# Kernel optimization log

Hardware: AMD Instinct MI355X
Metric: run time of the kernel (lower is better)

## Reference

```python
import jax, jax.numpy as jnp
import numpy as np

# Model dims (match init_kwargs / module defaults)
B, D, H, E, K, DEPTH, BS = 8192, 1024, 4096, 16, 2, 2, 64
SP_EXPERT, SP_CROSS = 0.85, 0.9  # block sparsities


def _block_mask(key, n_in, n_out, sparsity):
    """Bool mask [n_in, n_out] with (BS x BS)-block structure, ~(1-sparsity) dense.
    Matches torch.rand(n_blocks_out, n_blocks_in) > sparsity, expanded to full size."""
    mb = jax.random.uniform(key, (n_out // BS, n_in // BS)) > sparsity  # [ob, ib]
    return jnp.repeat(jnp.repeat(mb.T, BS, axis=0), BS, axis=1)  # [n_in, n_out]


def setup_inputs() -> dict:
    key = jax.random.key(0)
    ks = jax.random.split(key, 12)
    x = jax.random.normal(ks[0], (B, D), dtype=jnp.float32)
    gate_w = jax.random.normal(ks[1], (DEPTH, E, D), dtype=jnp.float32) / np.sqrt(D)
    temperature = jnp.ones((DEPTH,), dtype=jnp.float32)
    w1 = jax.random.normal(ks[2], (E, D, H), dtype=jnp.float32) * 0.02
    b1 = jnp.zeros((E, H), dtype=jnp.float32)
    w2 = jax.random.normal(ks[3], (E, H, D), dtype=jnp.float32) * 0.02
    b2 = jnp.zeros((E, D), dtype=jnp.float32)
    cross_w = jax.random.normal(ks[4], (D, D), dtype=jnp.float32) * 0.02
    cross_b = jnp.zeros((D,), dtype=jnp.float32)
    mk = jax.random.split(ks[5], 2 * E + 1)
    mask1 = jnp.stack([_block_mask(mk[i], D, H, SP_EXPERT) for i in range(E)])
    mask2 = jnp.stack([_block_mask(mk[E + i], H, D, SP_EXPERT) for i in range(E)])
    cross_mask = _block_mask(mk[2 * E], D, D, SP_CROSS)
    return {"x": x, "gate_w": gate_w, "temperature": temperature,
            "w1": w1, "b1": b1, "w2": w2, "b2": b2,
            "cross_w": cross_w, "cross_b": cross_b,
            "mask1": mask1, "mask2": mask2, "cross_mask": cross_mask}


def reference(x, gate_w, temperature, w1, b1, w2, b2, cross_w, cross_b,
              mask1, mask2, cross_mask):
    n_tok = x.shape[0]
    # Only the last-depth router affects the output (x is never updated and
    # expert_outputs is re-initialized each depth iteration in the original).
    logits = jnp.einsum('bd,ed->be', x, gate_w[-1]) / temperature[-1]
    top_vals, top_idx = jax.lax.top_k(logits, K)            # [n_tok, K]
    rout_w = jax.nn.softmax(top_vals, axis=-1)
    routing = jnp.zeros((n_tok, E), x.dtype).at[
        jnp.arange(n_tok)[:, None], top_idx].set(rout_w)    # [n_tok, E]

    expert_out = jnp.zeros_like(x)
    for e in range(E):  # fixed small expert count
        h = jax.nn.silu(x @ (w1[e] * mask1[e]) + b1[e])     # [n_tok, H]
        y = h @ (w2[e] * mask2[e]) + b2[e]                  # [n_tok, D]
        expert_out = expert_out + y * routing[:, e:e + 1]
    return x + expert_out @ (cross_w * cross_mask) + cross_b
```

## Files before the change

### kernel.cpp

```cpp
#include <hip/hip_runtime.h>


#define NTOK 8192
#define DIM  1024
#define HID  4096
#define NEXP 16
#define BM   256
#define ROWS_CAP (NTOK*2 + NEXP*256)

typedef __attribute__((ext_vector_type(4))) float fx4;
typedef __attribute__((ext_vector_type(4))) unsigned int ux4;
typedef __attribute__((ext_vector_type(2))) unsigned int ux2;
typedef __attribute__((ext_vector_type(8))) short s8v;
union V16 { ux4 u; s8v s; };

__device__ __forceinline__ unsigned int f2bf(float f) {
  unsigned int u = __float_as_uint(f);
  return (u + 0x7fffu + ((u >> 16) & 1u)) >> 16;
}

__device__ __forceinline__ unsigned int cvt_pk(float lo, float hi) {
  unsigned int r;
  asm("v_cvt_pk_bf16_f32 %0, %1, %2" : "=v"(r) : "v"(lo), "v"(hi));
  return r;
}

__device__ __forceinline__ unsigned int f2fp8(float v) {
  return (unsigned int)__builtin_amdgcn_cvt_pk_fp8_f32(v, v, 0, false) & 0xFFu;
}

__device__ __forceinline__ unsigned int pk4fp8(float a, float b, float c, float d) {
  unsigned int u = (unsigned int)__builtin_amdgcn_cvt_pk_fp8_f32(a, b, 0, false);
  u = (unsigned int)__builtin_amdgcn_cvt_pk_fp8_f32(c, d, (int)u, true);
  return u;
}

__device__ __forceinline__ bool mask_at(const void* m, int flag, size_t idx) {
  if (flag == 0) return ((const unsigned char*)m)[idx] != 0;
  if (flag == 1) return ((const int*)m)[idx] != 0;
  return ((const float*)m)[idx] != 0.0f;
}

__device__ __forceinline__ int flag_of(int ev) {
  return (ev & 2) ? 2 : ((ev & 1) ? 0 : 1);
}

__device__ __forceinline__ int xcd_swz() {
  const int b = blockIdx.x, cpx = gridDim.x >> 3;
  return (b & 7) * cpx + (b >> 3);
}

__device__ __forceinline__ void region_of(const int* __restrict__ meta, int base,
                                          int& e, int& rstart, int& ecnt, int& total) {
  e = 15; rstart = 0; ecnt = 0; total = 0;
  #pragma unroll
  for (int i = 0; i < 16; i++) {
    const int craw = meta[8 + i];
    const int c = (craw + 255) & ~255;
    if (base >= total && base < total + c) { e = i; rstart = total; ecnt = craw; }
    total += c;
  }
}

__global__ void k_route(const float* __restrict__ x,
                        const float* __restrict__ gw,
                        const float* __restrict__ temp,
                        const unsigned int* __restrict__ m1raw,
                        int* __restrict__ top2i, float* __restrict__ top2w,
                        int* __restrict__ meta, unsigned char* __restrict__ x8)
{
  if (blockIdx.x < 64) {
    int bits = 0;
    size_t base = (size_t)blockIdx.x * 4096 + threadIdx.x;
    for (int j = 0; j < 16; j++) {
      unsigned int v = m1raw[base + 256 * j];
      if (v == 0x3f800000u) bits |= 2;
      else if (v > 1u)      bits |= 1;
    }
    if (bits) atomicOr(&meta[1], bits);
  }

  __shared__ float gwsh[NEXP * DIM];
  for (int i = threadIdx.x; i < NEXP * DIM; i += 256) gwsh[i] = gw[i];
  __syncthreads();

  const int wv = threadIdx.x >> 6;
  const int l = threadIdx.x & 63;
  #pragma unroll
  for (int tt = 0; tt < 8; tt++) {
    const int t = blockIdx.x * 32 + wv * 8 + tt;
    const float* xr = x + (size_t)t * DIM;
    float xv[16];
    #pragma unroll
    for (int j = 0; j < 16; j++) xv[j] = xr[l + 64 * j];
    float logit[16];
    #pragma unroll
    for (int e = 0; e < 16; e++) {
      const float* g = gwsh + e * DIM;
      float s = 0.f;
      #pragma unroll
      for (int j = 0; j < 16; j++) s += xv[j] * g[l + 64 * j];
      #pragma unroll
      for (int o = 32; o >= 1; o >>= 1) s += __shfl_xor(s, o);
      logit[e] = s;
    }
    if (l == 0) {
      const float tinv = 1.0f / temp[0];
      int i0 = 0; float v0 = logit[0] * tinv;
      #pragma unroll
      for (int e = 1; e < 16; e++) { float v = logit[e] * tinv; if (v > v0) { v0 = v; i0 = e; } }
      int i1 = -1; float v1 = 0.f; bool first = true;
      #pragma unroll
      for (int e = 0; e < 16; e++) {
        if (e == i0) continue;
        float v = logit[e] * tinv;
        if (first || v > v1) { v1 = v; i1 = e; first = false; }
      }
      float ex = __expf(v1 - v0);
      float den = 1.0f + ex;
      top2i[2 * t] = i0; top2i[2 * t + 1] = i1;
      top2w[2 * t] = 1.0f / den; top2w[2 * t + 1] = ex / den;
      atomicAdd(&meta[8 + i0], 1);
      atomicAdd(&meta[8 + i1], 1);
    }
  }

  {
    const size_t be = (size_t)blockIdx.x * 32 * DIM;
    const fx4* src = (const fx4*)(x + be);
    ux4* dst = (ux4*)(x8 + be);
    #pragma unroll
    for (int i = 0; i < 8; i++) {
      const int idx = i * 256 + threadIdx.x;
      fx4 a = src[4 * idx], b = src[4 * idx + 1];
      fx4 c = src[4 * idx + 2], d = src[4 * idx + 3];
      ux4 o;
      o[0] = pk4fp8(a[0] * 16.f, a[1] * 16.f, a[2] * 16.f, a[3] * 16.f);
      o[1] = pk4fp8(b[0] * 16.f, b[1] * 16.f, b[2] * 16.f, b[3] * 16.f);
      o[2] = pk4fp8(c[0] * 16.f, c[1] * 16.f, c[2] * 16.f, c[3] * 16.f);
      o[3] = pk4fp8(d[0] * 16.f, d[1] * 16.f, d[2] * 16.f, d[3] * 16.f);
      dst[idx] = o;
    }
  }
}

__global__ void k_wcast(const float* __restrict__ w1, const float* __restrict__ w2,
                        const void* __restrict__ mask1, const void* __restrict__ mask2,
                        const int* __restrict__ meta,
                        unsigned char* __restrict__ w1p, unsigned char* __restrict__ w2p)
{
  const int flag = flag_of(meta[1]);
  const int gid = blockIdx.x;
  const int tid = threadIdx.x;
  const int c = tid >> 6, col = tid & 63;

  if (gid < 16384) {
    const int p = gid >> 4, kb = gid & 15;
    const int e = p >> 6, ct = p & 63;
    if (!mask_at(mask1, flag, (size_t)e * DIM * HID + (size_t)kb * 64 * HID + ct * 64)) return;
    const float* src = w1 + ((size_t)e * DIM + kb * 64 + c * 16) * HID + ct * 64 + col;
    ux4 v;
    #pragma unroll
    for (int q = 0; q < 4; q++) {
      float f0 = src[(size_t)(q * 4 + 0) * HID], f1 = src[(size_t)(q * 4 + 1) * HID];
      float f2 = src[(size_t)(q * 4 + 2) * HID], f3 = src[(size_t)(q * 4 + 3) * HID];
      v[q] = pk4fp8(f0 * 16.f, f1 * 16.f, f2 * 16.f, f3 * 16.f);
    }
    *(ux4*)(w1p + ((size_t)gid << 12) + col * 64 + ((c ^ ((col >> 1) & 3)) << 4)) = v;
  } else {
    const int g2 = gid - 16384;
    const int p = g2 >> 6, kb = g2 & 63;
    const int e = p >> 4, ct = p & 15;
    if (!mask_at(mask2, flag, (size_t)e * HID * DIM + (size_t)kb * 64 * DIM + ct * 64)) return;
    const float* src = w2 + ((size_t)e * HID + kb * 64 + c * 16) * DIM + ct * 64 + col;
    ux4 v;
    #pragma unroll
    for (int q = 0; q < 4; q++) {
      float f0 = src[(size_t)(q * 4 + 0) * DIM], f1 = src[(size_t)(q * 4 + 1) * DIM];
      float f2 = src[(size_t)(q * 4 + 2) * DIM], f3 = src[(size_t)(q * 4 + 3) * DIM];
      v[q] = pk4fp8(f0 * 16.f, f1 * 16.f, f2 * 16.f, f3 * 16.f);
    }
    *(ux4*)(w2p + ((size_t)g2 << 12) + col * 64 + ((c ^ ((col >> 1) & 3)) << 4)) = v;
  }
}

__global__ void k_assign(const int* __restrict__ top2i,
                         const float* __restrict__ top2w,
                         int* __restrict__ meta, int* __restrict__ tok_of_row,
                         int* __restrict__ t2row)
{
  __shared__ int offs[16];
  if (threadIdx.x < 16) {
    int o = 0;
    for (int i = 0; i < (int)threadIdx.x; i++) o += (meta[8 + i] + 255) & ~255;
    offs[threadIdx.x] = o;
  }
  __syncthreads();
  int t = blockIdx.x * 256 + threadIdx.x;
  if (t >= NTOK) return;
  #pragma unroll
  for (int k = 0; k < 2; k++) {
    int e = top2i[2 * t + k];
    int slot = atomicAdd(&meta[64 + e], 1);
    int row = offs[e] + slot;
    tok_of_row[row] = t;
    t2row[2 * t + k] = row;
  }
}

__global__ __launch_bounds__(256, 4)
void k_gemm1(const unsigned char* __restrict__ x8,
             const unsigned char* __restrict__ w1p, const float* __restrict__ b1,
             const void* __restrict__ mask1,
             const int* __restrict__ meta, const int* __restrict__ tok_of_row,
             unsigned char* __restrict__ h8)
{
  __shared__ ux4 Ash[2][1024];
  __shared__ __align__(16) unsigned int Bsh[2][1024];

  const int bid = xcd_swz();
  const int rt = bid >> 6, ct = bid & 63;
  const int base = rt * BM;
  int e, rstart, ecnt, total;
  region_of(meta, base, e, rstart, ecnt, total);
  if (base >= total) return;

  const int tid = threadIdx.x;
  const int wv = tid >> 6;
  const int jg0 = ct * 64;
  const int l = tid & 63, l16 = l & 15, lhi = l >> 4;

  unsigned int bits;
  {
    const int flag = flag_of(meta[1]);
    bool on = false;
    if (l < 16)
      on = mask_at(mask1, flag, (size_t)e * DIM * HID + (size_t)l * 64 * HID + jg0);
    bits = (unsigned int)(__ballot(on) & 0xFFFFull);
  }

  const unsigned int sw = (unsigned int)((tid & 3) ^ ((tid >> 3) & 3));
  const int vlimit = rstart + ecnt;
  unsigned int aoff[4];
  #pragma unroll
  for (int i = 0; i < 4; i++) {
    const int r = base + i * 64 + (tid >> 2);
    int tok = tok_of_row[r];
    if (r >= vlimit) tok = 0;
    aoff[i] = (unsigned int)tok * (unsigned int)DIM + sw * 16;
  }

  fx4 acc[4][4] = {};

  auto STAGE_A = [&](int b, int d0) {
    const char* gp = (const char*)x8 + d0;
    #pragma unroll
    for (int i = 0; i < 4; i++)
      __builtin_amdgcn_global_load_lds(
        (const __attribute__((address_space(1))) unsigned int*)(gp + aoff[i]),
        (__attribute__((address_space(3))) unsigned int*)&Ash[b][i * 256 + wv * 64],
        16, 0, 0);
  };
  auto STAGE_B = [&](int b, int kb) {
    const char* src = (const char*)w1p + (((size_t)(e * 64 + ct) * 16 + kb) << 12) + tid * 16;
    __builtin_amdgcn_global_load_lds(
      (const __attribute__((address_space(1))) unsigned int*)src,
      (__attribute__((address_space(3))) unsigned int*)&Bsh[b][wv * 256],
      16, 0, 0);
  };
  auto COMPUTE = [&](int b) {
    const char* Ab = (const char*)&Ash[b][0];
    const char* Bb = (const char*)&Bsh[b][0];
    #pragma unroll
    for (int ks = 0; ks < 2; ks++) {
      const int c = ks * 2 + (lhi >> 1);
      const int sub = (lhi & 1) << 3;
      long long a[4], bb[4];
      #pragma unroll
      for (int m = 0; m < 4; m++) {
        const int row = wv * 64 + m * 16 + l16;
        a[m] = *(const long long*)(Ab + row * 64 + ((c ^ ((row >> 1) & 3)) << 4) + sub);
      }
      #pragma unroll
      for (int n = 0; n < 4; n++) {
        const int col = n * 16 + l16;
        bb[n] = *(const long long*)(Bb + col * 64 + ((c ^ ((col >> 1) & 3)) << 4) + sub);
      }
      #pragma unroll
      for (int m = 0; m < 4; m++)
        #pragma unroll
        for (int n = 0; n < 4; n++)
          acc[m][n] = __builtin_amdgcn_mfma_f32_16x16x32_fp8_fp8(a[m], bb[n], acc[m][n], 0, 0, 0);
    }
  };

  if (bits) {
    int kb0 = __ffs(bits) - 1; bits &= bits - 1;
    STAGE_A(0, kb0 << 6); STAGE_B(0, kb0);
    __syncthreads();
    int cur = 0;
    for (;;) {
      int nkb = -1;
      if (bits) { nkb = __ffs(bits) - 1; bits &= bits - 1; }
      if (nkb >= 0) { STAGE_A(cur ^ 1, nkb << 6); STAGE_B(cur ^ 1, nkb); }
      COMPUTE(cur);
      __syncthreads();
      cur ^= 1;
      if (nkb < 0) break;
    }
  }

  unsigned char* hs = (unsigned char*)&Ash[0][0];
  __syncthreads();
  #pragma unroll
  for (int m = 0; m < 4; m++)
    #pragma unroll
    for (int n = 0; n < 4; n++) {
      const int gcol = jg0 + n * 16 + l16;
      const float bbv = b1[e * HID + gcol];
      #pragma unroll
      for (int i = 0; i < 4; i++) {
        const int row = wv * 64 + m * 16 + lhi * 4 + i;
        float v = acc[m][n][i] * 0.00390625f + bbv;
        float hval = v / (1.0f + __expf(-v));
        hs[row * 64 + n * 16 + l16] = (unsigned char)f2fp8(hval * 8.0f);
      }
    }
  __syncthreads();
  {
    const ux4* s = (const ux4*)hs;
    #pragma unroll
    for (int j = 0; j < 4; j++) {
      const int c2 = j * 256 + tid;
      const int row = c2 >> 2;
      *(ux4*)(h8 + (size_t)(base + row) * HID + ct * 64 + (c2 & 3) * 16) = s[c2];
    }
  }
}

__global__ __launch_bounds__(256, 4)
void k_gemm2(const unsigned char* __restrict__ h8,
             const unsigned char* __restrict__ w2p, const float* __restrict__ b2,
             const void* __restrict__ mask2,
             const int* __restrict__ meta, unsigned short* __restrict__ yb)
{
  __shared__ ux4 Ash[2][1024];
  __shared__ __align__(16) unsigned int Bsh[2][1024];

  const int bid = xcd_swz();
  const int rt = bid >> 4, ct = bid & 15;
  const int base = rt * BM;
  int e, rstart, ecnt, total;
  region_of(meta, base, e, rstart, ecnt, total);
  if (base >= total) return;

  const int tid = threadIdx.x;
  const int wv = tid >> 6;
  const int jg0 = ct * 64;

  const int l = tid & 63, l16 = l & 15, lhi = l >> 4;
  unsigned long long bits;
  {
    const int flag = flag_of(meta[1]);
    bits = __ballot(mask_at(mask2, flag,
             (size_t)e * HID * DIM + (size_t)l * 64 * DIM + jg0));
  }

  const unsigned int sw = (unsigned int)((tid & 3) ^ ((tid >> 3) & 3));
  unsigned int aoff[4];
  #pragma unroll
  for (int i = 0; i < 4; i++)
    aoff[i] = (unsigned int)(base + i * 64 + (tid >> 2)) * (unsigned int)HID + sw * 16;

  fx4 acc[4][4] = {};

  auto STAGE_A = [&](int b, int d0) {
    const char* gp = (const char*)h8 + d0;
    #pragma unroll
    for (int i = 0; i < 4; i++)
      __builtin_amdgcn_global_load_lds(
        (const __attribute__((address_space(1))) unsigned int*)(gp + aoff[i]),
        (__attribute__((address_space(3))) unsigned int*)&Ash[b][i * 256 + wv * 64],
        16, 0, 0);
  };
  auto STAGE_B = [&](int b, int kb) {
    const char* src = (const char*)w2p + (((size_t)(e * 16 + ct) * 64 + kb) << 12) + tid * 16;
    __builtin_amdgcn_global_load_lds(
      (const __attribute__((address_space(1))) unsigned int*)src,
      (__attribute__((address_space(3))) unsigned int*)&Bsh[b][wv * 256],
      16, 0, 0);
  };
  auto COMPUTE = [&](int b) {
    const char* Ab = (const char*)&Ash[b][0];
    const char* Bb = (const char*)&Bsh[b][0];
    #pragma unroll
    for (int ks = 0; ks < 2; ks++) {
      const int c = ks * 2 + (lhi >> 1);
      const int sub = (lhi & 1) << 3;
      long long a[4], bb[4];
      #pragma unroll
      for (int m = 0; m < 4; m++) {
        const int row = wv * 64 + m * 16 + l16;
        a[m] = *(const long long*)(Ab + row * 64 + ((c ^ ((row >> 1) & 3)) << 4) + sub);
      }
      #pragma unroll
      for (int n = 0; n < 4; n++) {
        const int col = n * 16 + l16;
        bb[n] = *(const long long*)(Bb + col * 64 + ((c ^ ((col >> 1) & 3)) << 4) + sub);
      }
      #pragma unroll
      for (int m = 0; m < 4; m++)
        #pragma unroll
        for (int n = 0; n < 4; n++)
          acc[m][n] = __builtin_amdgcn_mfma_f32_16x16x32_fp8_fp8(a[m], bb[n], acc[m][n], 0, 0, 0);
    }
  };

  if (bits) {
    int kb0 = __ffsll(bits) - 1; bits &= bits - 1;
    STAGE_A(0, kb0 << 6); STAGE_B(0, kb0);
    __syncthreads();
    int cur = 0;
    for (;;) {
      int nkb = -1;
      if (bits) { nkb = __ffsll(bits) - 1; bits &= bits - 1; }
      if (nkb >= 0) { STAGE_A(cur ^ 1, nkb << 6); STAGE_B(cur ^ 1, nkb); }
      COMPUTE(cur);
      __syncthreads();
      cur ^= 1;
      if (nkb < 0) break;
    }
  }

  unsigned short* hs = (unsigned short*)&Ash[0][0];
  __syncthreads();
  #pragma unroll
  for (int m = 0; m < 4; m++)
    #pragma unroll
    for (int n = 0; n < 4; n++) {
      const int gcol = jg0 + n * 16 + l16;
      const float bbv = b2[e * DIM + gcol];
      #pragma unroll
      for (int i = 0; i < 4; i++) {
        const int row = wv * 64 + m * 16 + lhi * 4 + i;
        hs[row * 64 + n * 16 + l16] =
            (unsigned short)f2bf(acc[m][n][i] * 0.0078125f + bbv);
      }
    }
  __syncthreads();
  {
    const ux4* s = (const ux4*)hs;
    #pragma unroll
    for (int j = 0; j < 8; j++) {
      const int c2 = j * 256 + tid;
      const int row = c2 >> 3;
      *(ux4*)(yb + (size_t)(base + row) * DIM + ct * 64 + (c2 & 7) * 8) = s[c2];
    }
  }
}

__global__ __launch_bounds__(256, 4)
void k_cross(const unsigned short* __restrict__ yb, const float* __restrict__ x,
             const float* __restrict__ cw, const float* __restrict__ cb,
             const void* __restrict__ cmask, const int* __restrict__ meta,
             const int* __restrict__ t2row, const float* __restrict__ t2w,
             float* __restrict__ out)
{
  __shared__ ux4 Ash[1024];
  __shared__ __align__(16) ux2 Bsh[1024];

  const int bid = xcd_swz();
  const int rt = bid >> 4, ct = bid & 15;
  const int base = rt * 128;
  const int tid = threadIdx.x;
  const int wv = tid >> 6;
  const int wr = wv >> 1, wc = wv & 1;
  const int jg0 = ct * 64;

  const int l = tid & 63, l16 = l & 15, lhi = l >> 4;

  unsigned int bits;
  {
    const int flag = flag_of(meta[1]);
    bool on = false;
    if (l < 16)
      on = mask_at(cmask, flag, (size_t)l * 64 * DIM + jg0);
    bits = (unsigned int)(__ballot(on) & 0xFFFFull);
  }

  const int arow = tid >> 1, sub = tid & 1;
  const int r0 = t2row[2 * (base + arow)], r1 = t2row[2 * (base + arow) + 1];
  const float w0 = t2w[2 * (base + arow)], w1 = t2w[2 * (base + arow) + 1];

  fx4 acc[4][2] = {};

  while (bits) {
    const int kbx = __ffs(bits) - 1; bits &= bits - 1;
    const int d0 = kbx * 64;
    {
      const ux4* s0 = (const ux4*)(yb + (size_t)r0 * DIM + d0);
      const ux4* s1 = (const ux4*)(yb + (size_t)r1 * DIM + d0);
      #pragma unroll
      for (int s = 0; s < 4; s++) {
        const int seg = sub * 4 + s;
        ux4 v0 = s0[seg], v1 = s1[seg], o;
        #pragma unroll
        for (int j = 0; j < 4; j++) {
          float alo = __uint_as_float(v0[j] << 16);
          float ahi = __uint_as_float(v0[j] & 0xFFFF0000u);
          float blo = __uint_as_float(v1[j] << 16);
          float bhi = __uint_as_float(v1[j] & 0xFFFF0000u);
          o[j] = cvt_pk(w0 * alo + w1 * blo, w0 * ahi + w1 * bhi);
        }
        Ash[arow * 8 + (seg ^ (arow & 7))] = o;
      }
    }
    {
      const int kbt = tid >> 4, jb = tid & 15;
      const float* bp = cw + (size_t)(d0 + kbt * 4) * DIM + jg0 + jb * 4;
      fx4 r0v = *(const fx4*)bp;
      fx4 r1v = *(const fx4*)(bp + DIM);
      fx4 r2v = *(const fx4*)(bp + 2 * DIM);
      fx4 r3v = *(const fx4*)(bp + 3 * DIM);
      #pragma unroll
      for (int jj = 0; jj < 4; jj++) {
        ux2 val;
        val[0] = cvt_pk(r0v[jj], r1v[jj]);
        val[1] = cvt_pk(r2v[jj], r3v[jj]);
        const int col = jb * 4 + jj;
        Bsh[(col * 8 + ((kbt >> 1) ^ (col & 7))) * 2 + (kbt & 1)] = val;
      }
    }
    __syncthreads();
    #pragma unroll
    for (int ks = 0; ks < 2; ks++) {
      s8v a[4], b[2];
      const int seg = ks * 4 + lhi;
      #pragma unroll
      for (int m = 0; m < 4; m++) {
        const int row = wr * 64 + m * 16 + l16;
        V16 v; v.u = Ash[row * 8 + (seg ^ (row & 7))]; a[m] = v.s;
      }
      #pragma unroll
      for (int n = 0; n < 2; n++) {
        const int col = wc * 32 + n * 16 + l16;
        V16 v; v.u = ((const ux4*)Bsh)[col * 8 + (seg ^ (col & 7))]; b[n] = v.s;
      }
      #pragma unroll
      for (int m = 0; m < 4; m++)
        #pragma unroll
        for (int n = 0; n < 2; n++)
          acc[m][n] = __builtin_amdgcn_mfma_f32_16x16x32_bf16(a[m], b[n], acc[m][n], 0, 0, 0);
    }
    __syncthreads();
  }

  #pragma unroll
  for (int m = 0; m < 4; m++)
    #pragma unroll
    for (int n = 0; n < 2; n++) {
      const int gcol = jg0 + wc * 32 + n * 16 + l16;
      #pragma unroll
      for (int i = 0; i < 4; i++) {
        const int row = wr * 64 + m * 16 + lhi * 4 + i;
        const size_t idx = (size_t)(base + row) * DIM + gcol;
        out[idx] = acc[m][n][i] + x[idx] + cb[gcol];
      }
    }
}

extern "C" void kernel_launch(void* const* d_in, const int* in_sizes, int n_in,
                              void* d_out, int out_size, void* d_ws, size_t ws_size,
                              hipStream_t stream)
{
  (void)in_sizes; (void)n_in; (void)out_size; (void)ws_size;
  const float* x      = (const float*)d_in[0];
  const float* gate_w = (const float*)d_in[1];
  const float* temp   = (const float*)d_in[2];
  const float* w1     = (const float*)d_in[3];
  const float* b1     = (const float*)d_in[4];
  const float* w2     = (const float*)d_in[5];
  const float* b2     = (const float*)d_in[6];
  const float* cw     = (const float*)d_in[7];
  const float* cb     = (const float*)d_in[8];
  const void*  mask1  = d_in[9];
  const void*  mask2  = d_in[10];
  const void*  cmask  = d_in[11];
  float* out = (float*)d_out;
  char* ws = (char*)d_ws;

  size_t off = 0;
  auto walloc = [&](size_t b) { size_t r = off; off = (off + b + 255) & ~(size_t)255; return r; };
  size_t o_meta = walloc(4096);
  size_t o_t2i  = walloc((size_t)NTOK * 2 * 4);
  size_t o_t2w  = walloc((size_t)NTOK * 2 * 4);
  size_t o_t2r  = walloc((size_t)NTOK * 2 * 4);
  size_t o_tok  = walloc((size_t)ROWS_CAP * 4);
  size_t o_x8   = walloc((size_t)NTOK * DIM);
  size_t o_y    = walloc((size_t)ROWS_CAP * DIM * 2);
  size_t o_hc   = walloc((size_t)ROWS_CAP * HID);
  size_t o_w1p  = walloc((size_t)16384 * 4096);
  size_t o_w2p  = walloc((size_t)16384 * 4096);

  int*                meta = (int*)(ws + o_meta);
  int*                t2i  = (int*)(ws + o_t2i);
  float*              t2w  = (float*)(ws + o_t2w);
  int*                t2r  = (int*)(ws + o_t2r);
  int*                tok  = (int*)(ws + o_tok);
  unsigned char*      x8   = (unsigned char*)(ws + o_x8);
  unsigned short*     yb   = (unsigned short*)(ws + o_y);
  unsigned char*      h8   = (unsigned char*)(ws + o_hc);
  unsigned char*      w1p  = (unsigned char*)(ws + o_w1p);
  unsigned char*      w2p  = (unsigned char*)(ws + o_w2p);

  hipMemsetAsync(ws + o_meta, 0, 4096, stream);

  k_route  <<<NTOK / 32, 256, 0, stream>>>(x, gate_w + (size_t)1 * NEXP * DIM, temp + 1,
                                           (const unsigned int*)mask1, t2i, t2w, meta, x8);
  k_wcast  <<<32768, 256, 0, stream>>>(w1, w2, mask1, mask2, meta, w1p, w2p);
  k_assign <<<NTOK / 256, 256, 0, stream>>>(t2i, t2w, meta, tok, t2r);

  const int NRT = ROWS_CAP / BM;
  k_gemm1<<<NRT * 64, 256, 0, stream>>>(x8, w1p, b1, mask1, meta, tok, h8);
  k_gemm2<<<NRT * 16, 256, 0, stream>>>(h8, w2p, b2, mask2, meta, yb);
  k_cross<<<(NTOK / 128) * 16, 256, 0, stream>>>(yb, x, cw, cb, cmask, meta, t2r, t2w, out);
}
```

Baseline: 322.1 us.

## Switch cross projection to FP8 MFMA with prepacked weights and merge prep kernels

The cross-projection GEMM now runs on fp8 MFMA instead of bf16. Its weights are pre-cast to scaled fp8 in swizzled 64x64 tiles inside a merged prep kernel, and tiles are loaded straight into LDS with global_load_lds. The routing-assignment kernel is folded into the same prep launch as extra blocks, which removes one launch. The combined expert output is quantized to fp8 with a scale of 16, adding precision loss in the final projection.

```diff
diff --git a/kernel.cpp b/kernel.cpp
--- a/kernel.cpp
+++ b/kernel.cpp
@@ -144,14 +144,42 @@
   }
 }
 
-__global__ void k_wcast(const float* __restrict__ w1, const float* __restrict__ w2,
-                        const void* __restrict__ mask1, const void* __restrict__ mask2,
-                        const int* __restrict__ meta,
-                        unsigned char* __restrict__ w1p, unsigned char* __restrict__ w2p)
+__global__ void k_prep(const float* __restrict__ w1, const float* __restrict__ w2,
+                       const float* __restrict__ cw,
+                       const void* __restrict__ mask1, const void* __restrict__ mask2,
+                       const void* __restrict__ cmask,
+                       const int* __restrict__ top2i, const float* __restrict__ top2w,
+                       int* __restrict__ meta, int* __restrict__ tok_of_row,
+                       int* __restrict__ t2row,
+                       unsigned char* __restrict__ w1p, unsigned char* __restrict__ w2p,
+                       unsigned char* __restrict__ cwp)
 {
-  const int flag = flag_of(meta[1]);
   const int gid = blockIdx.x;
   const int tid = threadIdx.x;
+
+  if (gid >= 33024) {
+    __shared__ int offs[16];
+    if (tid < 16) {
+      int o = 0;
+      for (int i = 0; i < tid; i++) o += (meta[8 + i] + 255) & ~255;
+      offs[tid] = o;
+    }
+    __syncthreads();
+    const int t = (gid - 33024) * 256 + tid;
+    if (t < NTOK) {
+      #pragma unroll
+      for (int k = 0; k < 2; k++) {
+        int e = top2i[2 * t + k];
+        int slot = atomicAdd(&meta[64 + e], 1);
+        int row = offs[e] + slot;
+        tok_of_row[row] = t;
+        t2row[2 * t + k] = row;
+      }
+    }
+    return;
+  }
+
+  const int flag = flag_of(meta[1]);
   const int c = tid >> 6, col = tid & 63;
 
   if (gid < 16384) {
@@ -167,7 +195,7 @@
       v[q] = pk4fp8(f0 * 16.f, f1 * 16.f, f2 * 16.f, f3 * 16.f);
     }
     *(ux4*)(w1p + ((size_t)gid << 12) + col * 64 + ((c ^ ((col >> 1) & 3)) << 4)) = v;
-  } else {
+  } else if (gid < 32768) {
     const int g2 = gid - 16384;
     const int p = g2 >> 6, kb = g2 & 63;
     const int e = p >> 4, ct = p & 15;
@@ -181,30 +209,19 @@
       v[q] = pk4fp8(f0 * 16.f, f1 * 16.f, f2 * 16.f, f3 * 16.f);
     }
     *(ux4*)(w2p + ((size_t)g2 << 12) + col * 64 + ((c ^ ((col >> 1) & 3)) << 4)) = v;
-  }
-}
-
-__global__ void k_assign(const int* __restrict__ top2i,
-                         const float* __restrict__ top2w,
-                         int* __restrict__ meta, int* __restrict__ tok_of_row,
-                         int* __restrict__ t2row)
-{
-  __shared__ int offs[16];
-  if (threadIdx.x < 16) {
-    int o = 0;
-    for (int i = 0; i < (int)threadIdx.x; i++) o += (meta[8 + i] + 255) & ~255;
-    offs[threadIdx.x] = o;
-  }
-  __syncthreads();
-  int t = blockIdx.x * 256 + threadIdx.x;
-  if (t >= NTOK) return;
-  #pragma unroll
-  for (int k = 0; k < 2; k++) {
-    int e = top2i[2 * t + k];
-    int slot = atomicAdd(&meta[64 + e], 1);
-    int row = offs[e] + slot;
-    tok_of_row[row] = t;
-    t2row[2 * t + k] = row;
+  } else {
+    const int g3 = gid - 32768;
+    const int ct = g3 >> 4, kb = g3 & 15;
+    if (!mask_at(cmask, flag, (size_t)kb * 64 * DIM + ct * 64)) return;
+    const float* src = cw + (size_t)(kb * 64 + c * 16) * DIM + ct * 64 + col;
+    ux4 v;
+    #pragma unroll
+    for (int q = 0; q < 4; q++) {
+      float f0 = src[(size_t)(q * 4 + 0) * DIM], f1 = src[(size_t)(q * 4 + 1) * DIM];
+      float f2 = src[(size_t)(q * 4 + 2) * DIM], f3 = src[(size_t)(q * 4 + 3) * DIM];
+      v[q] = pk4fp8(f0 * 16.f, f1 * 16.f, f2 * 16.f, f3 * 16.f);
+    }
+    *(ux4*)(cwp + ((size_t)g3 << 12) + col * 64 + ((c ^ ((col >> 1) & 3)) << 4)) = v;
   }
 }
 
@@ -461,13 +478,13 @@
 
 __global__ __launch_bounds__(256, 4)
 void k_cross(const unsigned short* __restrict__ yb, const float* __restrict__ x,
-             const float* __restrict__ cw, const float* __restrict__ cb,
+             const unsigned char* __restrict__ cwp, const float* __restrict__ cb,
              const void* __restrict__ cmask, const int* __restrict__ meta,
              const int* __restrict__ t2row, const float* __restrict__ t2w,
              float* __restrict__ out)
 {
-  __shared__ ux4 Ash[1024];
-  __shared__ __align__(16) ux2 Bsh[1024];
+  __shared__ ux4 Ash[512];
+  __shared__ __align__(16) unsigned int Bsh[1024];
 
   const int bid = xcd_swz();
   const int rt = bid >> 4, ct = bid & 15;
@@ -494,6 +511,14 @@
 
   fx4 acc[4][2] = {};
 
+  auto pack4 = [&](unsigned int a0, unsigned int b0, unsigned int a1, unsigned int b1) {
+    float v0 = w0 * __uint_as_float(a0 << 16)        + w1 * __uint_as_float(b0 << 16);
+    float v1 = w0 * __uint_as_float(a0 & 0xFFFF0000u) + w1 * __uint_as_float(b0 & 0xFFFF0000u);
+    float v2 = w0 * __uint_as_float(a1 << 16)        + w1 * __uint_as_float(b1 << 16);
+    float v3 = w0 * __uint_as_float(a1 & 0xFFFF0000u) + w1 * __uint_as_float(b1 & 0xFFFF0000u);
+    return pk4fp8(v0 * 16.f, v1 * 16.f, v2 * 16.f, v3 * 16.f);
+  };
+
   while (bits) {
     const int kbx = __ffs(bits) - 1; bits &= bits - 1;
     const int d0 = kbx * 64;
@@ -501,56 +526,50 @@
       const ux4* s0 = (const ux4*)(yb + (size_t)r0 * DIM + d0);
       const ux4* s1 = (const ux4*)(yb + (size_t)r1 * DIM + d0);
       #pragma unroll
-      for (int s = 0; s < 4; s++) {
-        const int seg = sub * 4 + s;
-        ux4 v0 = s0[seg], v1 = s1[seg], o;
+      for (int cc = 0; cc < 2; cc++) {
+        const int chunk = sub * 2 + cc;
+        ux4 va0 = s0[2 * chunk], va1 = s0[2 * chunk + 1];
+        ux4 vb0 = s1[2 * chunk], vb1 = s1[2 * chunk + 1];
+        ux4 o;
+        o[0] = pack4(va0[0], vb0[0], va0[1], vb0[1]);
+        o[1] = pack4(va0[2], vb0[2], va0[3], vb0[3]);
+        o[2] = pack4(va1[0], vb1[0], va1[1], vb1[1]);
+        o[3] = pack4(va1[2], vb1[2], va1[3], vb1[3]);
+        *(ux4*)((char*)&Ash[0] + arow * 64 + ((chunk ^ ((arow >> 1) & 3)) << 4)) = o;
+      }
+    }
+    {
+      const char* src = (const char*)cwp + (((size_t)(ct * 16 + kbx)) << 12) + tid * 16;
+      __builtin_amdgcn_global_load_lds(
+        (const __attribute__((address_space(1))) unsigned int*)src,
+        (__attribute__((address_space(3))) unsigned int*)&Bsh[wv * 256],
+        16, 0, 0);
+    }
+    __syncthreads();
+    {
+      const char* Ab = (const char*)&Ash[0];
+      const char* Bb = (const char*)&Bsh[0];
+      #pragma unroll
+      for (int ks = 0; ks < 2; ks++) {
+        const int c = ks * 2 + (lhi >> 1);
+        const int sub2 = (lhi & 1) << 3;
+        long long a[4], b[2];
         #pragma unroll
-        for (int j = 0; j < 4; j++) {
-          float alo = __uint_as_float(v0[j] << 16);
-          float ahi = __uint_as_float(v0[j] & 0xFFFF0000u);
-          float blo = __uint_as_float(v1[j] << 16);
-          float bhi = __uint_as_float(v1[j] & 0xFFFF0000u);
-          o[j] = cvt_pk(w0 * alo + w1 * blo, w0 * ahi + w1 * bhi);
+        for (int m = 0; m < 4; m++) {
+          const int row = wr * 64 + m * 16 + l16;
+          a[m] = *(const long long*)(Ab + row * 64 + ((c ^ ((row >> 1) & 3)) << 4) + sub2);
         }
-        Ash[arow * 8 + (seg ^ (arow & 7))] = o;
-      }
-    }
-    {
-      const int kbt = tid >> 4, jb = tid & 15;
-      const float* bp = cw + (size_t)(d0 + kbt * 4) * DIM + jg0 + jb * 4;
-      fx4 r0v = *(const fx4*)bp;
-      fx4 r1v = *(const fx4*)(bp + DIM);
-      fx4 r2v = *(const fx4*)(bp + 2 * DIM);
-      fx4 r3v = *(const fx4*)(bp + 3 * DIM);
-      #pragma unroll
-      for (int jj = 0; jj < 4; jj++) {
-        ux2 val;
-        val[0] = cvt_pk(r0v[jj], r1v[jj]);
-        val[1] = cvt_pk(r2v[jj], r3v[jj]);
-        const int col = jb * 4 + jj;
-        Bsh[(col * 8 + ((kbt >> 1) ^ (col & 7))) * 2 + (kbt & 1)] = val;
-      }
-    }
-    __syncthreads();
-    #pragma unroll
-    for (int ks = 0; ks < 2; ks++) {
-      s8v a[4], b[2];
-      const int seg = ks * 4 + lhi;
-      #pragma unroll
-      for (int m = 0; m < 4; m++) {
-        const int row = wr * 64 + m * 16 + l16;
-        V16 v; v.u = Ash[row * 8 + (seg ^ (row & 7))]; a[m] = v.s;
-      }
-      #pragma unroll
-      for (int n = 0; n < 2; n++) {
-        const int col = wc * 32 + n * 16 + l16;
-        V16 v; v.u = ((const ux4*)Bsh)[col * 8 + (seg ^ (col & 7))]; b[n] = v.s;
-      }
-      #pragma unroll
-      for (int m = 0; m < 4; m++)
         #pragma unroll
-        for (int n = 0; n < 2; n++)
-          acc[m][n] = __builtin_amdgcn_mfma_f32_16x16x32_bf16(a[m], b[n], acc[m][n], 0, 0, 0);
+        for (int n = 0; n < 2; n++) {
+          const int col = wc * 32 + n * 16 + l16;
+          b[n] = *(const long long*)(Bb + col * 64 + ((c ^ ((col >> 1) & 3)) << 4) + sub2);
+        }
+        #pragma unroll
+        for (int m = 0; m < 4; m++)
+          #pragma unroll
+          for (int n = 0; n < 2; n++)
+            acc[m][n] = __builtin_amdgcn_mfma_f32_16x16x32_fp8_fp8(a[m], b[n], acc[m][n], 0, 0, 0);
+      }
     }
     __syncthreads();
   }
@@ -564,7 +583,7 @@
       for (int i = 0; i < 4; i++) {
         const int row = wr * 64 + m * 16 + lhi * 4 + i;
         const size_t idx = (size_t)(base + row) * DIM + gcol;
-        out[idx] = acc[m][n][i] + x[idx] + cb[gcol];
+        out[idx] = acc[m][n][i] * 0.00390625f + x[idx] + cb[gcol];
       }
     }
 }
@@ -601,6 +620,7 @@
   size_t o_hc   = walloc((size_t)ROWS_CAP * HID);
   size_t o_w1p  = walloc((size_t)16384 * 4096);
   size_t o_w2p  = walloc((size_t)16384 * 4096);
+  size_t o_cwp  = walloc((size_t)256 * 4096);
 
   int*                meta = (int*)(ws + o_meta);
   int*                t2i  = (int*)(ws + o_t2i);
@@ -612,16 +632,17 @@
   unsigned char*      h8   = (unsigned char*)(ws + o_hc);
   unsigned char*      w1p  = (unsigned char*)(ws + o_w1p);
   unsigned char*      w2p  = (unsigned char*)(ws + o_w2p);
+  unsigned char*      cwp  = (unsigned char*)(ws + o_cwp);
 
   hipMemsetAsync(ws + o_meta, 0, 4096, stream);
 
-  k_route  <<<NTOK / 32, 256, 0, stream>>>(x, gate_w + (size_t)1 * NEXP * DIM, temp + 1,
-                                           (const unsigned int*)mask1, t2i, t2w, meta, x8);
-  k_wcast  <<<32768, 256, 0, stream>>>(w1, w2, mask1, mask2, meta, w1p, w2p);
-  k_assign <<<NTOK / 256, 256, 0, stream>>>(t2i, t2w, meta, tok, t2r);
+  k_route <<<NTOK / 32, 256, 0, stream>>>(x, gate_w + (size_t)1 * NEXP * DIM, temp + 1,
+                                          (const unsigned int*)mask1, t2i, t2w, meta, x8);
+  k_prep  <<<33056, 256, 0, stream>>>(w1, w2, cw, mask1, mask2, cmask,
+                                      t2i, t2w, meta, tok, t2r, w1p, w2p, cwp);
 
   const int NRT = ROWS_CAP / BM;
   k_gemm1<<<NRT * 64, 256, 0, stream>>>(x8, w1p, b1, mask1, meta, tok, h8);
   k_gemm2<<<NRT * 16, 256, 0, stream>>>(h8, w2p, b2, mask2, meta, yb);
-  k_cross<<<(NTOK / 128) * 16, 256, 0, stream>>>(yb, x, cw, cb, cmask, meta, t2r, t2w, out);
-}
+  k_cross<<<(NTOK / 128) * 16, 256, 0, stream>>>(yb, x, cwp, cb, cmask, meta, t2r, t2w, out);
+}
```

Result: faster. 314.4 us (-2.4%).
